# Kernel optimization log

Hardware: AMD Instinct MI355X
Metric: run time of the kernel (lower is better)

Reference implementation:

```python
import jax, jax.numpy as jnp
import numpy as np

NUM_CLOTHES = 50000
FEAT_DIM = 256
BATCH = 1024
MOMENTUM = 0.0
SCALE = 16.0
EPSILON = 0.1


def setup_inputs() -> dict:
    key = jax.random.key(0)
    k1, k2, k3, k4 = jax.random.split(key, 4)
    inputs = jax.random.normal(k1, (BATCH, FEAT_DIM), dtype=jnp.float32)
    feature_memory = jax.random.normal(k2, (NUM_CLOTHES, FEAT_DIM), dtype=jnp.float32)
    targets = jax.random.randint(k3, (BATCH,), 0, NUM_CLOTHES, dtype=jnp.int64)
    # binary positive mask; guarantee the identity (own-clothes) column is positive
    positive_mask = (jax.random.uniform(k4, (BATCH, NUM_CLOTHES)) < 0.01).astype(jnp.float32)
    positive_mask = positive_mask.at[jnp.arange(BATCH), targets].set(1.0)
    return {"inputs": inputs, "feature_memory": feature_memory,
            "positive_mask": positive_mask, "targets": targets}


def _l2_normalize(x, axis=-1):
    # matches F.normalize(p=2): divide by max(||x||, 1e-12)
    n = jnp.sqrt(jnp.sum(x * x, axis=axis, keepdims=True))
    return x / jnp.maximum(n, 1e-12)


def reference(inputs, feature_memory, positive_mask, targets):
    B = inputs.shape[0]
    # ---- memory update: scatter-mean of detached features per clothes label ----
    feats = jax.lax.stop_gradient(inputs)
    sums = jax.ops.segment_sum(feats, targets, num_segments=NUM_CLOTHES)      # [C, D]
    counts = jax.ops.segment_sum(jnp.ones((B,), feats.dtype), targets,
                                 num_segments=NUM_CLOTHES)                     # [C]
    mean = sums / jnp.maximum(counts, 1.0)[:, None]
    present = (counts > 0)[:, None]
    memory = jnp.where(present,
                       MOMENTUM * feature_memory + (1.0 - MOMENTUM) * mean,
                       feature_memory)                                         # [C, D]
    memory = jax.lax.stop_gradient(memory)
    # ---- similarities against memory bank ----
    inputs_norm = _l2_normalize(inputs)
    memory_norm = _l2_normalize(memory)
    similarities = jnp.einsum('bd,cd->bc', inputs_norm, memory_norm) * SCALE   # [B, C]
    # ---- masked log-sum-exp loss ----
    negative_mask = 1.0 - positive_mask
    mask_identity = jax.nn.one_hot(targets, NUM_CLOTHES, dtype=similarities.dtype)
    exp_logits = jnp.exp(similarities)
    neg_sum = jnp.sum(exp_logits * negative_mask, axis=1, keepdims=True)       # [B, 1]
    log_prob = similarities - jnp.log(neg_sum + exp_logits)
    pos_count = jnp.sum(positive_mask, axis=1, keepdims=True)
    mask = (1.0 - EPSILON) * mask_identity + (EPSILON / pos_count) * positive_mask
    loss = jnp.mean(jnp.sum(-mask * log_prob, axis=1))
    return loss
```

## Files before the change

kernel.cpp:

```cpp
#include <hip/hip_runtime.h>
#include <hip/hip_bf16.h>
#include <stdint.h>

#define NCLOTHES 50000
#define CPAD     50048
#define NCB      391
#define NCB2     782
#define FDIM     256
#define NBATCH   1024
#define SCALEF   16.0f
#define EPSW     0.1f
#define SLOTS    8

typedef __attribute__((ext_vector_type(8))) short short8;
typedef __attribute__((ext_vector_type(4))) float f32x4;

__device__ __forceinline__ void gload_lds16(const void* gsrc, void* ldst) {
    __builtin_amdgcn_global_load_lds(
        (const __attribute__((address_space(1))) void*)gsrc,
        (__attribute__((address_space(3))) void*)ldst, 16, 0, 0);
}

__global__ void anorm_kernel(const float* __restrict__ in, __hip_bfloat16* __restrict__ A) {
    int b = blockIdx.x, t = threadIdx.x;
    float x = in[b * FDIM + t];
    float ss = x * x;
    #pragma unroll
    for (int o = 32; o > 0; o >>= 1) ss += __shfl_xor(ss, o);
    __shared__ float sh[4];
    if ((t & 63) == 0) sh[t >> 6] = ss;
    __syncthreads();
    float tot = sh[0] + sh[1] + sh[2] + sh[3];
    float r = SCALEF / fmaxf(sqrtf(tot), 1e-12f);
    A[b * FDIM + t] = __float2bfloat16(x * r);
}

__global__ __launch_bounds__(256)
void bnorm_all(const float* __restrict__ fm, __hip_bfloat16* __restrict__ Bm) {
    const int nw = (gridDim.x * 256) >> 6;
    int w = (blockIdx.x * 256 + threadIdx.x) >> 6;
    int lane = threadIdx.x & 63;
    for (int row = w; row < CPAD; row += nw) {
        __hip_bfloat16 h[4];
        if (row >= NCLOTHES) {
            h[0] = h[1] = h[2] = h[3] = __float2bfloat16(0.f);
        } else {
            f32x4 v = *(const f32x4*)(fm + (size_t)row * FDIM + lane * 4);
            float ss = v.x * v.x + v.y * v.y + v.z * v.z + v.w * v.w;
            #pragma unroll
            for (int o = 32; o > 0; o >>= 1) ss += __shfl_xor(ss, o);
            float r = 1.f / fmaxf(sqrtf(ss), 1e-12f);
            h[0] = __float2bfloat16(v.x * r);
            h[1] = __float2bfloat16(v.y * r);
            h[2] = __float2bfloat16(v.z * r);
            h[3] = __float2bfloat16(v.w * r);
        }
        *(ushort4*)(Bm + (size_t)row * FDIM + lane * 4) = *(const ushort4*)h;
    }
}

__global__ void bnorm_present(const float* __restrict__ in, const int* __restrict__ tg,
                              __hip_bfloat16* __restrict__ Bm) {
    int b = blockIdx.x, t = threadIdx.x;
    __shared__ int stg[NBATCH];
    #pragma unroll
    for (int j = 0; j < 4; ++j) stg[t + j * 256] = tg[t + j * 256];
    __syncthreads();
    int c = stg[b];
    bool dup = false;
    #pragma unroll
    for (int j = 0; j < 4; ++j) {
        int i = t + j * 256;
        if (i < b && stg[i] == c) dup = true;
    }
    if (__syncthreads_or(dup)) return;
    __shared__ int mlist[64];
    __shared__ int mcount;
    if (t == 0) mcount = 0;
    __syncthreads();
    #pragma unroll
    for (int j = 0; j < 4; ++j) {
        int i = t + j * 256;
        if (stg[i] == c) { int p = atomicAdd(&mcount, 1); if (p < 64) mlist[p] = i; }
    }
    __syncthreads();
    int n = mcount;
    float v = 0.f;
    for (int i = 0; i < n; ++i) v += in[mlist[i] * FDIM + t];
    v /= (float)n;
    float ss = v * v;
    #pragma unroll
    for (int o = 32; o > 0; o >>= 1) ss += __shfl_xor(ss, o);
    __shared__ float sh[4];
    if ((t & 63) == 0) sh[t >> 6] = ss;
    __syncthreads();
    float tot = sh[0] + sh[1] + sh[2] + sh[3];
    float r = 1.0f / fmaxf(sqrtf(tot), 1e-12f);
    Bm[(size_t)c * FDIM + t] = __float2bfloat16(v * r);
}

#define BM 128
#define BN 128
#define BK 32
#define NKSTEP (FDIM / BK)

__global__ __launch_bounds__(256, 4)
void gemm_kernel(const __hip_bfloat16* __restrict__ A, const __hip_bfloat16* __restrict__ Bm,
                 const float* __restrict__ pm,
                 float* __restrict__ partial_ns,
                 unsigned int* __restrict__ cnt,
                 float* __restrict__ sbuf,
                 unsigned char* __restrict__ colbuf)
{
    __shared__ alignas(16) __hip_bfloat16 As[2][BM * BK];
    __shared__ alignas(16) __hip_bfloat16 Bs[2][BM * BK];

    const int t = threadIdx.x;
    const int bx = blockIdx.x;
    const int bn0 = bx * BN;
    const int bm0 = blockIdx.y * BM;

    const int lane = t & 63;
    const int wave = t >> 6;
    const int wr = wave >> 1, wc = wave & 1;
    const int lrow = lane & 15, lq = lane >> 4;

    const int sr = t >> 2;
    const int sk = (t & 3) * 8;

    f32x4 acc[4][4];
    #pragma unroll
    for (int m = 0; m < 4; ++m)
        #pragma unroll
        for (int n = 0; n < 4; ++n) acc[m][n] = (f32x4)0.f;

    {
        const __hip_bfloat16* ag = A + (size_t)(bm0 + sr) * FDIM + sk;
        const __hip_bfloat16* bg = Bm + (size_t)(bn0 + sr) * FDIM + sk;
        gload_lds16(ag,             (void*)&As[0][t * 8]);
        gload_lds16(ag + 64 * FDIM, (void*)&As[0][2048 + t * 8]);
        gload_lds16(bg,             (void*)&Bs[0][t * 8]);
        gload_lds16(bg + 64 * FDIM, (void*)&Bs[0][2048 + t * 8]);
    }

    for (int ks = 0; ks < NKSTEP; ++ks) {
        __syncthreads();
        int cur = ks & 1;
        if (ks + 1 < NKSTEP) {
            int nxt = cur ^ 1;
            int k0 = (ks + 1) * BK;
            const __hip_bfloat16* ag = A + (size_t)(bm0 + sr) * FDIM + k0 + sk;
            const __hip_bfloat16* bg = Bm + (size_t)(bn0 + sr) * FDIM + k0 + sk;
            gload_lds16(ag,             (void*)&As[nxt][t * 8]);
            gload_lds16(ag + 64 * FDIM, (void*)&As[nxt][2048 + t * 8]);
            gload_lds16(bg,             (void*)&Bs[nxt][t * 8]);
            gload_lds16(bg + 64 * FDIM, (void*)&Bs[nxt][2048 + t * 8]);
        }
        short8 af[4], bf[4];
        #pragma unroll
        for (int m = 0; m < 4; ++m)
            af[m] = *(const short8*)&As[cur][(wr * 64 + m * 16 + lrow) * BK + lq * 8];
        #pragma unroll
        for (int n = 0; n < 4; ++n)
            bf[n] = *(const short8*)&Bs[cur][(wc * 64 + n * 16 + lrow) * BK + lq * 8];
        #pragma unroll
        for (int m = 0; m < 4; ++m)
            #pragma unroll
            for (int n = 0; n < 4; ++n)
                acc[m][n] = __builtin_amdgcn_mfma_f32_16x16x32_bf16(af[m], bf[n], acc[m][n], 0, 0, 0);
    }

    const int cb2 = bx * 2 + wc;
    const int colbase = bn0 + wc * 64;

    #pragma unroll
    for (int m = 0; m < 4; ++m) {
        #pragma unroll
        for (int r = 0; r < 4; ++r) {
            const int grow = bm0 + wr * 64 + m * 16 + lq * 4 + r;
            const float* prow = pm + (size_t)grow * NCLOTHES + colbase + lrow;
            float pv[4];
            #pragma unroll
            for (int n = 0; n < 4; ++n) pv[n] = prow[n * 16];
            float pneg = 0.f;
            unsigned posn = 0;
            #pragma unroll
            for (int n = 0; n < 4; ++n) {
                bool valid = (colbase + n * 16 + lrow) < NCLOTHES;
                bool pos = valid && (pv[n] >= 0.5f);
                if (pos) posn |= (1u << n);
                pneg += (valid && !pos) ? __expf(acc[m][n][r]) : 0.f;
            }
            pneg += __shfl_xor(pneg, 1);
            pneg += __shfl_xor(pneg, 2);
            pneg += __shfl_xor(pneg, 4);
            pneg += __shfl_xor(pneg, 8);
            const size_t idx = (size_t)grow * NCB2 + cb2;
            int slot_base = 0;
            #pragma unroll
            for (int n = 0; n < 4; ++n) {
                unsigned long long bal = __ballot((posn >> n) & 1);
                unsigned seg = (unsigned)((bal >> (lq * 16)) & 0xFFFFull);
                int pre = slot_base + __popc(seg & ((1u << lrow) - 1u));
                if (((posn >> n) & 1) && pre < SLOTS) {
                    sbuf[idx * SLOTS + pre] = acc[m][n][r];
                    colbuf[idx * SLOTS + pre] = (unsigned char)(n * 16 + lrow);
                }
                slot_base += __popc(seg);
            }
            if (lrow == 0) {
                cnt[idx] = (unsigned int)(slot_base < SLOTS ? slot_base : SLOTS);
                partial_ns[idx] = pneg;
            }
        }
    }
}

__global__ void finish_kernel(const float* __restrict__ partial_ns, const unsigned int* __restrict__ cnt,
                              const float* __restrict__ sbuf, const unsigned char* __restrict__ colbuf,
                              const int* __restrict__ tg, float* __restrict__ loss_rows) {
    int b = blockIdx.x, t = threadIdx.x;
    int tgt = tg[b];
    float ns = 0.f;
    int np = 0;
    for (int cb = t; cb < NCB2; cb += 256) {
        size_t idx = (size_t)b * NCB2 + cb;
        ns += partial_ns[idx];
        np += (int)cnt[idx];
    }
    #pragma unroll
    for (int o = 32; o > 0; o >>= 1) { ns += __shfl_xor(ns, o); np += __shfl_xor(np, o); }
    __shared__ float shn[4]; __shared__ int shp[4];
    if ((t & 63) == 0) { shn[t >> 6] = ns; shp[t >> 6] = np; }
    __syncthreads();
    ns = shn[0] + shn[1] + shn[2] + shn[3];
    np = shp[0] + shp[1] + shp[2] + shp[3];

    float slp = 0.f, idlp = 0.f;
    for (int cb = t; cb < NCB2; cb += 256) {
        size_t idx = (size_t)b * NCB2 + cb;
        int k = (int)cnt[idx];
        for (int i = 0; i < k; ++i) {
            float s = sbuf[idx * SLOTS + i];
            int col = cb * 64 + (int)colbuf[idx * SLOTS + i];
            float lp = s - __logf(ns + __expf(s));
            slp += lp;
            if (col == tgt) idlp += lp;
        }
    }
    #pragma unroll
    for (int o = 32; o > 0; o >>= 1) { slp += __shfl_xor(slp, o); idlp += __shfl_xor(idlp, o); }
    __shared__ float sh1[4], sh2[4];
    if ((t & 63) == 0) { sh1[t >> 6] = slp; sh2[t >> 6] = idlp; }
    __syncthreads();
    if (t == 0) {
        float s_all = sh1[0] + sh1[1] + sh1[2] + sh1[3];
        float i_all = sh2[0] + sh2[1] + sh2[2] + sh2[3];
        loss_rows[b] = -((1.0f - EPSW) * i_all + (EPSW / (float)np) * s_all);
    }
}

__global__ void reduce_kernel(const float* __restrict__ lr, float* __restrict__ out) {
    int t = threadIdx.x;
    float s = lr[t] + lr[t + 256] + lr[t + 512] + lr[t + 768];
    #pragma unroll
    for (int o = 32; o > 0; o >>= 1) s += __shfl_xor(s, o);
    __shared__ float sh[4];
    if ((t & 63) == 0) sh[t >> 6] = s;
    __syncthreads();
    if (t == 0) out[0] = (sh[0] + sh[1] + sh[2] + sh[3]) * (1.0f / NBATCH);
}

extern "C" void kernel_launch(void* const* d_in, const int* in_sizes, int n_in,
                              void* d_out, int out_size, void* d_ws, size_t ws_size,
                              hipStream_t stream) {
    const float* inputs  = (const float*)d_in[0];
    const float* fm      = (const float*)d_in[1];
    const float* pmask   = (const float*)d_in[2];
    const int*   targets = (const int*)d_in[3];
    float* out = (float*)d_out;

    char* ws = (char*)d_ws;
    size_t off = 0;
    __hip_bfloat16* A = (__hip_bfloat16*)(ws + off);  off += (size_t)NBATCH * FDIM * 2;
    __hip_bfloat16* Bm = (__hip_bfloat16*)(ws + off); off += (size_t)CPAD * FDIM * 2;
    off = (off + 255) & ~(size_t)255;
    float* partial_ns = (float*)(ws + off);        off += (size_t)NBATCH * NCB2 * 4;
    unsigned int* cnt = (unsigned int*)(ws + off); off += (size_t)NBATCH * NCB2 * 4;
    float* sbuf = (float*)(ws + off);              off += (size_t)NBATCH * NCB2 * SLOTS * 4;
    unsigned char* colbuf = (unsigned char*)(ws + off); off += (size_t)NBATCH * NCB2 * SLOTS;
    off = (off + 255) & ~(size_t)255;
    float* loss_rows = (float*)(ws + off);         off += 4096;

    anorm_kernel<<<NBATCH, 256, 0, stream>>>(inputs, A);
    bnorm_all<<<2048, 256, 0, stream>>>(fm, Bm);
    bnorm_present<<<NBATCH, 256, 0, stream>>>(inputs, targets, Bm);
    gemm_kernel<<<dim3(NCB, NBATCH / BM), 256, 0, stream>>>(A, Bm, pmask, partial_ns, cnt, sbuf, colbuf);
    finish_kernel<<<NBATCH, 256, 0, stream>>>(partial_ns, cnt, sbuf, colbuf, targets, loss_rows);
    reduce_kernel<<<1, 256, 0, stream>>>(loss_rows, out);
}
```

Measured before the change: 411.7 us.

## Drop LDS staging in GEMM, load MFMA fragments directly and prefetch mask

Removes the double-buffered LDS tiles and barriers, so each wave loads its bf16 A/B fragments straight from global memory (relying on L2 for reuse). Part of the positive-mask reads is issued before the MFMA loop and the rest right after it, so mask loads overlap with compute instead of sitting serially in the epilogue. Occupancy hint drops from 4 to 3 blocks per CU to make room for the extra registers. The risk is more global and L2 traffic and uncoalesced 16-byte fragment loads in place of shared-memory reuse across waves.

```diff
diff --git a/kernel.cpp b/kernel.cpp
--- a/kernel.cpp
+++ b/kernel.cpp
@@ -4,7 +4,6 @@
 
 #define NCLOTHES 50000
 #define CPAD     50048
-#define NCB      391
 #define NCB2     782
 #define FDIM     256
 #define NBATCH   1024
@@ -14,12 +13,6 @@
 
 typedef __attribute__((ext_vector_type(8))) short short8;
 typedef __attribute__((ext_vector_type(4))) float f32x4;
-
-__device__ __forceinline__ void gload_lds16(const void* gsrc, void* ldst) {
-    __builtin_amdgcn_global_load_lds(
-        (const __attribute__((address_space(1))) void*)gsrc,
-        (__attribute__((address_space(3))) void*)ldst, 16, 0, 0);
-}
 
 __global__ void anorm_kernel(const float* __restrict__ in, __hip_bfloat16* __restrict__ A) {
     int b = blockIdx.x, t = threadIdx.x;
@@ -99,12 +92,7 @@
     Bm[(size_t)c * FDIM + t] = __float2bfloat16(v * r);
 }
 
-#define BM 128
-#define BN 128
-#define BK 32
-#define NKSTEP (FDIM / BK)
-
-__global__ __launch_bounds__(256, 4)
+__global__ __launch_bounds__(256, 3)
 void gemm_kernel(const __hip_bfloat16* __restrict__ A, const __hip_bfloat16* __restrict__ Bm,
                  const float* __restrict__ pm,
                  float* __restrict__ partial_ns,
@@ -112,21 +100,30 @@
                  float* __restrict__ sbuf,
                  unsigned char* __restrict__ colbuf)
 {
-    __shared__ alignas(16) __hip_bfloat16 As[2][BM * BK];
-    __shared__ alignas(16) __hip_bfloat16 Bs[2][BM * BK];
-
     const int t = threadIdx.x;
-    const int bx = blockIdx.x;
-    const int bn0 = bx * BN;
-    const int bm0 = blockIdx.y * BM;
-
     const int lane = t & 63;
     const int wave = t >> 6;
     const int wr = wave >> 1, wc = wave & 1;
     const int lrow = lane & 15, lq = lane >> 4;
 
-    const int sr = t >> 2;
-    const int sk = (t & 3) * 8;
+    const int rowbase = blockIdx.y * 128 + wr * 64;
+    const int colbase = blockIdx.x * 128 + wc * 64;
+    const int cb2 = blockIdx.x * 2 + wc;
+
+    const float* pmw = pm + (size_t)rowbase * NCLOTHES + colbase;
+    const __hip_bfloat16* Ab = A  + (size_t)rowbase * FDIM + lq * 8;
+    const __hip_bfloat16* Bb = Bm + (size_t)colbase * FDIM + lq * 8;
+
+    bool vld[4];
+    #pragma unroll
+    for (int n = 0; n < 4; ++n) vld[n] = (colbase + n * 16 + lrow) < NCLOTHES;
+
+    float pv0[4][4];
+    #pragma unroll
+    for (int r = 0; r < 4; ++r)
+        #pragma unroll
+        for (int n = 0; n < 4; ++n)
+            pv0[r][n] = vld[n] ? pmw[(size_t)(lq * 4 + r) * NCLOTHES + n * 16 + lrow] : 0.f;
 
     f32x4 acc[4][4];
     #pragma unroll
@@ -134,35 +131,15 @@
         #pragma unroll
         for (int n = 0; n < 4; ++n) acc[m][n] = (f32x4)0.f;
 
-    {
-        const __hip_bfloat16* ag = A + (size_t)(bm0 + sr) * FDIM + sk;
-        const __hip_bfloat16* bg = Bm + (size_t)(bn0 + sr) * FDIM + sk;
-        gload_lds16(ag,             (void*)&As[0][t * 8]);
-        gload_lds16(ag + 64 * FDIM, (void*)&As[0][2048 + t * 8]);
-        gload_lds16(bg,             (void*)&Bs[0][t * 8]);
-        gload_lds16(bg + 64 * FDIM, (void*)&Bs[0][2048 + t * 8]);
-    }
-
-    for (int ks = 0; ks < NKSTEP; ++ks) {
-        __syncthreads();
-        int cur = ks & 1;
-        if (ks + 1 < NKSTEP) {
-            int nxt = cur ^ 1;
-            int k0 = (ks + 1) * BK;
-            const __hip_bfloat16* ag = A + (size_t)(bm0 + sr) * FDIM + k0 + sk;
-            const __hip_bfloat16* bg = Bm + (size_t)(bn0 + sr) * FDIM + k0 + sk;
-            gload_lds16(ag,             (void*)&As[nxt][t * 8]);
-            gload_lds16(ag + 64 * FDIM, (void*)&As[nxt][2048 + t * 8]);
-            gload_lds16(bg,             (void*)&Bs[nxt][t * 8]);
-            gload_lds16(bg + 64 * FDIM, (void*)&Bs[nxt][2048 + t * 8]);
-        }
+    #pragma unroll 2
+    for (int ks = 0; ks < FDIM / 32; ++ks) {
         short8 af[4], bf[4];
         #pragma unroll
         for (int m = 0; m < 4; ++m)
-            af[m] = *(const short8*)&As[cur][(wr * 64 + m * 16 + lrow) * BK + lq * 8];
+            af[m] = *(const short8*)(Ab + (size_t)(m * 16 + lrow) * FDIM + ks * 32);
         #pragma unroll
         for (int n = 0; n < 4; ++n)
-            bf[n] = *(const short8*)&Bs[cur][(wc * 64 + n * 16 + lrow) * BK + lq * 8];
+            bf[n] = *(const short8*)(Bb + (size_t)(n * 16 + lrow) * FDIM + ks * 32);
         #pragma unroll
         for (int m = 0; m < 4; ++m)
             #pragma unroll
@@ -170,26 +147,30 @@
                 acc[m][n] = __builtin_amdgcn_mfma_f32_16x16x32_bf16(af[m], bf[n], acc[m][n], 0, 0, 0);
     }
 
-    const int cb2 = bx * 2 + wc;
-    const int colbase = bn0 + wc * 64;
+    float pv1[4][4], pv2[4][4], pv3[4][4];
+    #pragma unroll
+    for (int r = 0; r < 4; ++r)
+        #pragma unroll
+        for (int n = 0; n < 4; ++n) {
+            int col = n * 16 + lrow;
+            pv1[r][n] = vld[n] ? pmw[(size_t)(16 + lq * 4 + r) * NCLOTHES + col] : 0.f;
+            pv2[r][n] = vld[n] ? pmw[(size_t)(32 + lq * 4 + r) * NCLOTHES + col] : 0.f;
+            pv3[r][n] = vld[n] ? pmw[(size_t)(48 + lq * 4 + r) * NCLOTHES + col] : 0.f;
+        }
 
     #pragma unroll
     for (int m = 0; m < 4; ++m) {
         #pragma unroll
         for (int r = 0; r < 4; ++r) {
-            const int grow = bm0 + wr * 64 + m * 16 + lq * 4 + r;
-            const float* prow = pm + (size_t)grow * NCLOTHES + colbase + lrow;
-            float pv[4];
-            #pragma unroll
-            for (int n = 0; n < 4; ++n) pv[n] = prow[n * 16];
+            const int grow = rowbase + m * 16 + lq * 4 + r;
             float pneg = 0.f;
             unsigned posn = 0;
             #pragma unroll
             for (int n = 0; n < 4; ++n) {
-                bool valid = (colbase + n * 16 + lrow) < NCLOTHES;
-                bool pos = valid && (pv[n] >= 0.5f);
+                float pmv = (m == 0) ? pv0[r][n] : (m == 1) ? pv1[r][n] : (m == 2) ? pv2[r][n] : pv3[r][n];
+                bool pos = vld[n] && (pmv >= 0.5f);
                 if (pos) posn |= (1u << n);
-                pneg += (valid && !pos) ? __expf(acc[m][n][r]) : 0.f;
+                pneg += (vld[n] && !pos) ? __expf(acc[m][n][r]) : 0.f;
             }
             pneg += __shfl_xor(pneg, 1);
             pneg += __shfl_xor(pneg, 2);
@@ -295,7 +276,7 @@
     anorm_kernel<<<NBATCH, 256, 0, stream>>>(inputs, A);
     bnorm_all<<<2048, 256, 0, stream>>>(fm, Bm);
     bnorm_present<<<NBATCH, 256, 0, stream>>>(inputs, targets, Bm);
-    gemm_kernel<<<dim3(NCB, NBATCH / BM), 256, 0, stream>>>(A, Bm, pmask, partial_ns, cnt, sbuf, colbuf);
+    gemm_kernel<<<dim3(CPAD / 128, NBATCH / 128), 256, 0, stream>>>(A, Bm, pmask, partial_ns, cnt, sbuf, colbuf);
     finish_kernel<<<NBATCH, 256, 0, stream>>>(partial_ns, cnt, sbuf, colbuf, targets, loss_rows);
     reduce_kernel<<<1, 256, 0, stream>>>(loss_rows, out);
 }
```

Result: slower. 475.0 us (+15.4%).

## Pre-pack positive mask into bitwords and read them in GEMM epilogue

Applied to the files above, without the earlier changes.

Adds a pack kernel that turns the fp32 positive mask into 64-bit ballot words per row, one word per 64 columns. The GEMM epilogue reads one word per row instead of strided fp32 mask loads, and derives slot positions with popcount rather than cross-lane ballots. Per-block count and column buffers are dropped, and partial_ns/sbuf are laid out column-block-major. The full mask is still read once in the pack kernel, and the extra launch plus the finish kernel now re-reading the mask words add some overhead.

```diff
diff --git a/kernel.cpp b/kernel.cpp
--- a/kernel.cpp
+++ b/kernel.cpp
@@ -4,7 +4,7 @@
 
 #define NCLOTHES 50000
 #define CPAD     50048
-#define NCB      391
+#define NWORDS   782
 #define NCB2     782
 #define FDIM     256
 #define NBATCH   1024
@@ -99,6 +99,36 @@
     Bm[(size_t)c * FDIM + t] = __float2bfloat16(v * r);
 }
 
+__global__ __launch_bounds__(256)
+void pack_kernel(const float* __restrict__ pm, unsigned long long* __restrict__ maskw) {
+    const int row = blockIdx.x;
+    const int half = blockIdx.y;
+    const int wave = threadIdx.x >> 6;
+    const int lane = threadIdx.x & 63;
+    const float* prow = pm + (size_t)row * NCLOTHES;
+    unsigned long long* wrow = maskw + (size_t)row * NWORDS;
+    for (int chunk = half * 98 + wave; chunk < half * 98 + 98; chunk += 4) {
+        int base = chunk * 256;
+        unsigned long long b0, b1, b2, b3;
+        {
+            int c0 = base + lane;
+            float v0 = (c0 < NCLOTHES) ? prow[c0] : 0.f;
+            float v1 = (c0 + 64 < NCLOTHES) ? prow[c0 + 64] : 0.f;
+            float v2 = (c0 + 128 < NCLOTHES) ? prow[c0 + 128] : 0.f;
+            float v3 = (c0 + 192 < NCLOTHES) ? prow[c0 + 192] : 0.f;
+            b0 = __ballot(v0 >= 0.5f);
+            b1 = __ballot(v1 >= 0.5f);
+            b2 = __ballot(v2 >= 0.5f);
+            b3 = __ballot(v3 >= 0.5f);
+        }
+        if (lane < 4) {
+            int wi = chunk * 4 + lane;
+            unsigned long long w = (lane == 0) ? b0 : (lane == 1) ? b1 : (lane == 2) ? b2 : b3;
+            if (wi < NWORDS) wrow[wi] = w;
+        }
+    }
+}
+
 #define BM 128
 #define BN 128
 #define BK 32
@@ -106,11 +136,9 @@
 
 __global__ __launch_bounds__(256, 4)
 void gemm_kernel(const __hip_bfloat16* __restrict__ A, const __hip_bfloat16* __restrict__ Bm,
-                 const float* __restrict__ pm,
+                 const unsigned long long* __restrict__ maskw,
                  float* __restrict__ partial_ns,
-                 unsigned int* __restrict__ cnt,
-                 float* __restrict__ sbuf,
-                 unsigned char* __restrict__ colbuf)
+                 float* __restrict__ sbuf)
 {
     __shared__ alignas(16) __hip_bfloat16 As[2][BM * BK];
     __shared__ alignas(16) __hip_bfloat16 Bs[2][BM * BK];
@@ -170,93 +198,103 @@
                 acc[m][n] = __builtin_amdgcn_mfma_f32_16x16x32_bf16(af[m], bf[n], acc[m][n], 0, 0, 0);
     }
 
+    const int rowbase = bm0 + wr * 64;
+    const int colbase = bn0 + wc * 64;
     const int cb2 = bx * 2 + wc;
-    const int colbase = bn0 + wc * 64;
+
+    unsigned long long mwv[4][4];
+    #pragma unroll
+    for (int m = 0; m < 4; ++m)
+        #pragma unroll
+        for (int r = 0; r < 4; ++r) {
+            int grow = rowbase + m * 16 + lq * 4 + r;
+            mwv[m][r] = maskw[(size_t)grow * NWORDS + cb2];
+        }
 
     #pragma unroll
     for (int m = 0; m < 4; ++m) {
         #pragma unroll
         for (int r = 0; r < 4; ++r) {
-            const int grow = bm0 + wr * 64 + m * 16 + lq * 4 + r;
-            const float* prow = pm + (size_t)grow * NCLOTHES + colbase + lrow;
-            float pv[4];
-            #pragma unroll
-            for (int n = 0; n < 4; ++n) pv[n] = prow[n * 16];
+            const int grow = rowbase + m * 16 + lq * 4 + r;
+            const unsigned long long mw = mwv[m][r];
             float pneg = 0.f;
-            unsigned posn = 0;
             #pragma unroll
             for (int n = 0; n < 4; ++n) {
-                bool valid = (colbase + n * 16 + lrow) < NCLOTHES;
-                bool pos = valid && (pv[n] >= 0.5f);
-                if (pos) posn |= (1u << n);
-                pneg += (valid && !pos) ? __expf(acc[m][n][r]) : 0.f;
+                const int p = n * 16 + lrow;
+                bool vld = (colbase + p) < NCLOTHES;
+                bool pos = (mw >> p) & 1ull;
+                pneg += (vld && !pos) ? __expf(acc[m][n][r]) : 0.f;
             }
             pneg += __shfl_xor(pneg, 1);
             pneg += __shfl_xor(pneg, 2);
             pneg += __shfl_xor(pneg, 4);
             pneg += __shfl_xor(pneg, 8);
-            const size_t idx = (size_t)grow * NCB2 + cb2;
-            int slot_base = 0;
+            const size_t base = ((size_t)cb2 * NBATCH + grow);
             #pragma unroll
             for (int n = 0; n < 4; ++n) {
-                unsigned long long bal = __ballot((posn >> n) & 1);
-                unsigned seg = (unsigned)((bal >> (lq * 16)) & 0xFFFFull);
-                int pre = slot_base + __popc(seg & ((1u << lrow) - 1u));
-                if (((posn >> n) & 1) && pre < SLOTS) {
-                    sbuf[idx * SLOTS + pre] = acc[m][n][r];
-                    colbuf[idx * SLOTS + pre] = (unsigned char)(n * 16 + lrow);
+                const int p = n * 16 + lrow;
+                if ((mw >> p) & 1ull) {
+                    int pre = __popcll(mw & ((1ull << p) - 1ull));
+                    if (pre < SLOTS) sbuf[base * SLOTS + pre] = acc[m][n][r];
                 }
-                slot_base += __popc(seg);
             }
-            if (lrow == 0) {
-                cnt[idx] = (unsigned int)(slot_base < SLOTS ? slot_base : SLOTS);
-                partial_ns[idx] = pneg;
-            }
-        }
-    }
-}
-
-__global__ void finish_kernel(const float* __restrict__ partial_ns, const unsigned int* __restrict__ cnt,
-                              const float* __restrict__ sbuf, const unsigned char* __restrict__ colbuf,
+            if (lrow == 0) partial_ns[base] = pneg;
+        }
+    }
+}
+
+__global__ void finish_kernel(const float* __restrict__ partial_ns,
+                              const unsigned long long* __restrict__ maskw,
+                              const float* __restrict__ sbuf,
                               const int* __restrict__ tg, float* __restrict__ loss_rows) {
     int b = blockIdx.x, t = threadIdx.x;
     int tgt = tg[b];
+    const int cbt = tgt >> 6, bitp = tgt & 63;
+
     float ns = 0.f;
+    for (int cb = t; cb < NCB2; cb += 256) ns += partial_ns[(size_t)cb * NBATCH + b];
+    #pragma unroll
+    for (int o = 32; o > 0; o >>= 1) ns += __shfl_xor(ns, o);
+    __shared__ float shn[4];
+    if ((t & 63) == 0) shn[t >> 6] = ns;
+    __syncthreads();
+    ns = shn[0] + shn[1] + shn[2] + shn[3];
+
+    float slp = 0.f, idlp = 0.f;
     int np = 0;
     for (int cb = t; cb < NCB2; cb += 256) {
-        size_t idx = (size_t)b * NCB2 + cb;
-        ns += partial_ns[idx];
-        np += (int)cnt[idx];
-    }
-    #pragma unroll
-    for (int o = 32; o > 0; o >>= 1) { ns += __shfl_xor(ns, o); np += __shfl_xor(np, o); }
-    __shared__ float shn[4]; __shared__ int shp[4];
-    if ((t & 63) == 0) { shn[t >> 6] = ns; shp[t >> 6] = np; }
-    __syncthreads();
-    ns = shn[0] + shn[1] + shn[2] + shn[3];
-    np = shp[0] + shp[1] + shp[2] + shp[3];
-
-    float slp = 0.f, idlp = 0.f;
-    for (int cb = t; cb < NCB2; cb += 256) {
-        size_t idx = (size_t)b * NCB2 + cb;
-        int k = (int)cnt[idx];
-        for (int i = 0; i < k; ++i) {
-            float s = sbuf[idx * SLOTS + i];
-            int col = cb * 64 + (int)colbuf[idx * SLOTS + i];
-            float lp = s - __logf(ns + __expf(s));
-            slp += lp;
-            if (col == tgt) idlp += lp;
-        }
-    }
-    #pragma unroll
-    for (int o = 32; o > 0; o >>= 1) { slp += __shfl_xor(slp, o); idlp += __shfl_xor(idlp, o); }
+        unsigned long long mw = maskw[(size_t)b * NWORDS + cb];
+        int k = __popcll(mw);
+        np += k;
+        int kk = k < SLOTS ? k : SLOTS;
+        const float* sp = sbuf + ((size_t)cb * NBATCH + b) * SLOTS;
+        for (int i = 0; i < kk; ++i) {
+            float s = sp[i];
+            slp += s - __logf(ns + __expf(s));
+        }
+        if (cb == cbt) {
+            int idslot = __popcll(mw & ((1ull << bitp) - 1ull));
+            if (idslot < SLOTS) {
+                float s = sp[idslot];
+                idlp = s - __logf(ns + __expf(s));
+            }
+        }
+    }
+    #pragma unroll
+    for (int o = 32; o > 0; o >>= 1) {
+        slp += __shfl_xor(slp, o);
+        idlp += __shfl_xor(idlp, o);
+        np += __shfl_xor(np, o);
+    }
     __shared__ float sh1[4], sh2[4];
-    if ((t & 63) == 0) { sh1[t >> 6] = slp; sh2[t >> 6] = idlp; }
+    __shared__ int shp[4];
+    if ((t & 63) == 0) { sh1[t >> 6] = slp; sh2[t >> 6] = idlp; shp[t >> 6] = np; }
     __syncthreads();
     if (t == 0) {
         float s_all = sh1[0] + sh1[1] + sh1[2] + sh1[3];
         float i_all = sh2[0] + sh2[1] + sh2[2] + sh2[3];
-        loss_rows[b] = -((1.0f - EPSW) * i_all + (EPSW / (float)np) * s_all);
+        int np_all = shp[0] + shp[1] + shp[2] + shp[3];
+        loss_rows[b] = -((1.0f - EPSW) * i_all + (EPSW / (float)np_all) * s_all);
     }
 }
 
@@ -285,17 +323,17 @@
     __hip_bfloat16* A = (__hip_bfloat16*)(ws + off);  off += (size_t)NBATCH * FDIM * 2;
     __hip_bfloat16* Bm = (__hip_bfloat16*)(ws + off); off += (size_t)CPAD * FDIM * 2;
     off = (off + 255) & ~(size_t)255;
-    float* partial_ns = (float*)(ws + off);        off += (size_t)NBATCH * NCB2 * 4;
-    unsigned int* cnt = (unsigned int*)(ws + off); off += (size_t)NBATCH * NCB2 * 4;
-    float* sbuf = (float*)(ws + off);              off += (size_t)NBATCH * NCB2 * SLOTS * 4;
-    unsigned char* colbuf = (unsigned char*)(ws + off); off += (size_t)NBATCH * NCB2 * SLOTS;
+    unsigned long long* maskw = (unsigned long long*)(ws + off); off += (size_t)NBATCH * NWORDS * 8;
+    float* partial_ns = (float*)(ws + off);        off += (size_t)NCB2 * NBATCH * 4;
+    float* sbuf = (float*)(ws + off);              off += (size_t)NCB2 * NBATCH * SLOTS * 4;
     off = (off + 255) & ~(size_t)255;
     float* loss_rows = (float*)(ws + off);         off += 4096;
 
     anorm_kernel<<<NBATCH, 256, 0, stream>>>(inputs, A);
     bnorm_all<<<2048, 256, 0, stream>>>(fm, Bm);
     bnorm_present<<<NBATCH, 256, 0, stream>>>(inputs, targets, Bm);
-    gemm_kernel<<<dim3(NCB, NBATCH / BM), 256, 0, stream>>>(A, Bm, pmask, partial_ns, cnt, sbuf, colbuf);
-    finish_kernel<<<NBATCH, 256, 0, stream>>>(partial_ns, cnt, sbuf, colbuf, targets, loss_rows);
+    pack_kernel<<<dim3(NBATCH, 2), 256, 0, stream>>>(pmask, maskw);
+    gemm_kernel<<<dim3(CPAD / BN, NBATCH / BM), 256, 0, stream>>>(A, Bm, maskw, partial_ns, sbuf);
+    finish_kernel<<<NBATCH, 256, 0, stream>>>(partial_ns, maskw, sbuf, targets, loss_rows);
     reduce_kernel<<<1, 256, 0, stream>>>(loss_rows, out);
 }
```

Result: slower. 469.1 us (+13.9%).
